# Optimization experiments

Hardware: AMD Instinct MI355X
Metric: run time of the kernel (lower is better)

## Reference

```python
import jax, jax.numpy as jnp
import numpy as np


def setup_inputs() -> dict:
    key = jax.random.key(0)
    k1, k2 = jax.random.split(key)
    latent = jax.random.normal(k1, (131072, 128), dtype=jnp.float32)
    coords = jax.random.normal(k2, (2048, 128), dtype=jnp.float32)
    return {"latent": latent, "coords": coords}


def reference(latent, coords):
    # torch.cdist(latent, coords).min(1)[1]
    # argmin over euclidean distance == argmin over squared distance,
    # so we skip the sqrt (same result, cheaper and numerically safer).
    x2 = jnp.sum(latent * latent, axis=1, keepdims=True)          # [N, 1]
    c2 = jnp.sum(coords * coords, axis=1)                          # [C]
    cross = latent @ coords.T                                      # [N, C]
    d2 = x2 + c2[None, :] - 2.0 * cross                            # [N, C] squared dists
    return jnp.argmin(d2, axis=1)                                  # [N] int indices
```

## Files before the change

kernel.cpp:

```cpp
#include <hip/hip_runtime.h>


constexpr int D = 128;
constexpr int C = 2048;
constexpr int NCH = 32;
constexpr int NCHUNKS = C / NCH;
constexpr float MARGIN_H = 0.01f;
constexpr int WL_CAP = 32768;

constexpr size_t WS_CNT = 16384;
constexpr size_t WS_WL  = 32768;
constexpr size_t WS_BH  = 262144;
constexpr size_t WS_BL  = 524288;

typedef __attribute__((ext_vector_type(4))) int   i32x4;
typedef unsigned int u32;

__device__ __forceinline__ int pack4(int a0, int a1, int a2, int a3) {
    return (int)(((u32)a0 & 255u) | (((u32)a1 & 255u) << 8) |
                 (((u32)a2 & 255u) << 16) | (((u32)a3 & 255u) << 24));
}

__device__ __forceinline__ void q2(float v, float qa, float inv, float inv128,
                                   int* h, int* l) {
    float hf = __builtin_rintf(v * inv);
    *h = (int)hf;
    float r = fmaf(-hf, qa, v);
    *l = (int)__builtin_rintf(r * inv128);
}

__device__ __forceinline__ void gl_lds16(const void* g, void* l) {
    __builtin_amdgcn_global_load_lds(
        (const __attribute__((address_space(1))) u32*)g,
        (__attribute__((address_space(3))) u32*)l, 16, 0, 0);
}

__global__ void prep_coords(const float* __restrict__ coords,
                            signed char* __restrict__ Bh,
                            signed char* __restrict__ Bl,
                            float2* __restrict__ qc2, int* __restrict__ counter) {
    int t = blockIdx.x * blockDim.x + threadIdx.x;
    if (t == 0) *counter = 0;
    if (t >= C * 4) return;
    int c = t >> 2, p = t & 3;
    float v[32];
#pragma unroll
    for (int i = 0; i < 8; ++i)
        *(float4*)(v + i * 4) = *(const float4*)(coords + (size_t)c * D + p * 32 + i * 4);
    float amax = 0.f, ss = 0.f;
#pragma unroll
    for (int j = 0; j < 32; ++j) {
        amax = fmaxf(amax, fabsf(v[j]));
        ss = fmaf(v[j], v[j], ss);
    }
#pragma unroll
    for (int m = 1; m <= 2; m <<= 1) {
        amax = fmaxf(amax, __shfl_xor(amax, m, 64));
        ss += __shfl_xor(ss, m, 64);
    }
    float qb = fmaxf(amax, 1e-30f) * (1.f / 127.f);
    float inv = 127.f / fmaxf(amax, 1e-30f);
    float inv128 = inv * 128.f;

#pragma unroll
    for (int g = 0; g < 2; ++g) {
        int g8 = p * 2 + g;
        int hw[4], lw[4];
#pragma unroll
        for (int w = 0; w < 4; ++w) {
            int h0, l0, h1, l1, h2, l2, h3, l3;
            q2(v[g * 16 + w * 4 + 0], qb, inv, inv128, &h0, &l0);
            q2(v[g * 16 + w * 4 + 1], qb, inv, inv128, &h1, &l1);
            q2(v[g * 16 + w * 4 + 2], qb, inv, inv128, &h2, &l2);
            q2(v[g * 16 + w * 4 + 3], qb, inv, inv128, &h3, &l3);
            hw[w] = pack4(h0, h1, h2, h3);
            lw[w] = pack4(l0, l1, l2, l3);
        }
        size_t off = (size_t)c * 128 + (size_t)((g8 ^ (c & 7)) * 16);
        *(i32x4*)(Bh + off) = (i32x4){hw[0], hw[1], hw[2], hw[3]};
        *(i32x4*)(Bl + off) = (i32x4){lw[0], lw[1], lw[2], lw[3]};
    }
    if (p == 0) qc2[c] = make_float2(qb, -0.5f * ss);
}


__global__ __launch_bounds__(256, 4) void centroid_fast(
        const float* __restrict__ latent,
        const signed char* __restrict__ Bh_img,
        const signed char* __restrict__ Bl_img,
        const float2* __restrict__ qc2g,
        int* __restrict__ out,
        int* __restrict__ counter,
        int* __restrict__ worklist) {
    __shared__ __align__(16) signed char Bh[2][NCH * 128], Bl[2][NCH * 128];
    __shared__ __align__(16) float2 sqc[C];

    const int tid  = threadIdx.x;
    const int wid  = tid >> 6;
    const int lane = tid & 63;
    const int q    = lane >> 4, lr = lane & 15;
    const int row_block = blockIdx.x * 64;

    {
        int ph = (blockIdx.x ^ (blockIdx.x >> 8)) & 3;
        for (int i = 0; i < ph * 2; ++i) __builtin_amdgcn_s_sleep(8);
    }

    gl_lds16(Bh_img + tid * 16, &Bh[0][tid * 16]);
    gl_lds16(Bl_img + tid * 16, &Bl[0][tid * 16]);
#pragma unroll
    for (int i = 0; i < 4; ++i) {
        int off = (i * 256 + tid) * 16;
        gl_lds16((const char*)qc2g + off, (char*)sqc + off);
    }

    i32x4 Ah[2], Al[2];
    float qAr[4];
    {
        const float* rp = latent + (size_t)(row_block + wid * 16 + lr) * D;
        float v[32];
#pragma unroll
        for (int ks = 0; ks < 2; ++ks)
#pragma unroll
            for (int i = 0; i < 4; ++i)
                *(float4*)(v + ks * 16 + i * 4) =
                    *(const float4*)(rp + ks * 64 + q * 16 + i * 4);
        float amax = 0.f;
#pragma unroll
        for (int j = 0; j < 32; ++j) amax = fmaxf(amax, fabsf(v[j]));
        amax = fmaxf(amax, __shfl_xor(amax, 16, 64));
        amax = fmaxf(amax, __shfl_xor(amax, 32, 64));
        float qa = fmaxf(amax, 1e-30f) * (1.f / 127.f);
        float inv = 127.f / fmaxf(amax, 1e-30f);
        float inv128 = inv * 128.f;
#pragma unroll
        for (int ks = 0; ks < 2; ++ks) {
            int hw[4], lw[4];
#pragma unroll
            for (int w = 0; w < 4; ++w) {
                int h0, l0, h1, l1, h2, l2, h3, l3;
                q2(v[ks * 16 + w * 4 + 0], qa, inv, inv128, &h0, &l0);
                q2(v[ks * 16 + w * 4 + 1], qa, inv, inv128, &h1, &l1);
                q2(v[ks * 16 + w * 4 + 2], qa, inv, inv128, &h2, &l2);
                q2(v[ks * 16 + w * 4 + 3], qa, inv, inv128, &h3, &l3);
                hw[w] = pack4(h0, h1, h2, h3);
                lw[w] = pack4(l0, l1, l2, l3);
            }
            Ah[ks] = (i32x4){hw[0], hw[1], hw[2], hw[3]};
            Al[ks] = (i32x4){lw[0], lw[1], lw[2], lw[3]};
        }
#pragma unroll
        for (int r = 0; r < 4; ++r)
            qAr[r] = __shfl(qa, (lane & 48) | (q * 4 + r), 64);
    }

    float b1[4], b2[4];
    int   bidx[4];
#pragma unroll
    for (int s = 0; s < 4; ++s) { b1[s] = -3.4e38f; b2[s] = -3.4e38f; bidx[s] = 0; }

    __syncthreads();

    for (int ch = 0; ch < NCHUNKS; ++ch) {
        const int buf = ch & 1;
        const int chbase = ch * NCH;
        if (ch + 1 < NCHUNKS) {
            const signed char* sh = Bh_img + (size_t)(ch + 1) * (NCH * 128);
            const signed char* sl = Bl_img + (size_t)(ch + 1) * (NCH * 128);
            gl_lds16(sh + tid * 16, &Bh[buf ^ 1][tid * 16]);
            gl_lds16(sl + tid * 16, &Bl[buf ^ 1][tid * 16]);
            asm volatile("s_waitcnt vmcnt(2)" ::: "memory");
        } else {
            asm volatile("s_waitcnt vmcnt(0)" ::: "memory");
        }
        __builtin_amdgcn_s_barrier();

#pragma unroll
        for (int nt = 0; nt < 2; ++nt) {
            const int nl = nt * 16 + lr;
            const float2 qc = sqc[chbase + nl];
            i32x4 I1 = (i32x4){0, 0, 0, 0};
            i32x4 I2 = (i32x4){0, 0, 0, 0};
            __builtin_amdgcn_s_setprio(1);
#pragma unroll
            for (int ks = 0; ks < 2; ++ks) {
                const int e = nl * 128 + (((ks << 2) | q) ^ (lr & 7)) * 16;
                i32x4 bh = *(const i32x4*)(&Bh[buf][e]);
                i32x4 bl = *(const i32x4*)(&Bl[buf][e]);
                I1 = __builtin_amdgcn_mfma_i32_16x16x64_i8(Ah[ks], bh, I1, 0, 0, 0);
                I2 = __builtin_amdgcn_mfma_i32_16x16x64_i8(Ah[ks], bl, I2, 0, 0, 0);
                I2 = __builtin_amdgcn_mfma_i32_16x16x64_i8(Al[ks], bh, I2, 0, 0, 0);
            }
            __builtin_amdgcn_s_setprio(0);
            const int n_global = chbase + nl;
#pragma unroll
            for (int r = 0; r < 4; ++r) {
                float x = fmaf((float)I2[r], 0.0078125f, (float)I1[r]);
                float a = fmaf(qAr[r], x * qc.x, qc.y);
                b2[r]   = __builtin_amdgcn_fmed3f(a, b1[r], b2[r]);
                bool gt = a > b1[r];
                b1[r]   = fmaxf(a, b1[r]);
                bidx[r] = gt ? n_global : bidx[r];
            }
        }
        __builtin_amdgcn_s_barrier();
    }

#pragma unroll
    for (int m = 1; m <= 8; m <<= 1) {
#pragma unroll
        for (int s = 0; s < 4; ++s) {
            float oa = __shfl_xor(b1[s], m, 64);
            float ob = __shfl_xor(b2[s], m, 64);
            int   oi = __shfl_xor(bidx[s], m, 64);
            float mn = fminf(b1[s], oa);
            b2[s] = fmaxf(fmaxf(b2[s], ob), mn);
            bool take = oa > b1[s];
            b1[s]   = take ? oa : b1[s];
            bidx[s] = take ? oi : bidx[s];
        }
    }
#pragma unroll
    for (int s = 0; s < 4; ++s) {
        if (lr == s) {
            int row = row_block + wid * 16 + q * 4 + s;
            out[row] = bidx[s];
            if (b1[s] - b2[s] < MARGIN_H) {
                int w = atomicAdd(counter, 1);
                if (w < WL_CAP) worklist[w] = row;
            }
        }
    }
}


__global__ __launch_bounds__(1024) void refine_fp64(
        const float* __restrict__ latent, const float* __restrict__ coords,
        const int* __restrict__ worklist, const int* __restrict__ counter,
        int wl_cap, int* __restrict__ out) {
    __shared__ float  xs[D];
    __shared__ double rv[1024];
    __shared__ int    ri[1024];

    int n = *counter;
    if (n > wl_cap) n = wl_cap;

    for (int wi = blockIdx.x; wi < n; wi += gridDim.x) {
        int row = worklist[wi];
        if (threadIdx.x < D)
            xs[threadIdx.x] = latent[(size_t)row * D + threadIdx.x];
        __syncthreads();

        double best = 1.0e300;
        int    bix  = 0;
        for (int c = threadIdx.x; c < C; c += 1024) {
            const float4* cp = (const float4*)(coords + (size_t)c * D);
            double s0 = 0.0, s1 = 0.0, s2 = 0.0, s3 = 0.0;
#pragma unroll 8
            for (int k4 = 0; k4 < 32; ++k4) {
                float4 v = cp[k4];
                double d0 = (double)xs[k4 * 4 + 0] - (double)v.x;
                double d1 = (double)xs[k4 * 4 + 1] - (double)v.y;
                double d2 = (double)xs[k4 * 4 + 2] - (double)v.z;
                double d3 = (double)xs[k4 * 4 + 3] - (double)v.w;
                s0 = fma(d0, d0, s0); s1 = fma(d1, d1, s1);
                s2 = fma(d2, d2, s2); s3 = fma(d3, d3, s3);
            }
            double s = (s0 + s1) + (s2 + s3);
            if (s < best) { best = s; bix = c; }
        }
        rv[threadIdx.x] = best;
        ri[threadIdx.x] = bix;
        __syncthreads();
        for (int off = 512; off > 0; off >>= 1) {
            if (threadIdx.x < off) {
                double ov = rv[threadIdx.x + off];
                int    oi = ri[threadIdx.x + off];
                if (ov < rv[threadIdx.x] ||
                    (ov == rv[threadIdx.x] && oi < ri[threadIdx.x])) {
                    rv[threadIdx.x] = ov;
                    ri[threadIdx.x] = oi;
                }
            }
            __syncthreads();
        }
        if (threadIdx.x == 0) out[row] = ri[0];
        __syncthreads();
    }
}

extern "C" void kernel_launch(void* const* d_in, const int* in_sizes, int n_in,
                              void* d_out, int out_size, void* d_ws, size_t ws_size,
                              hipStream_t stream) {
    const float* latent = (const float*)d_in[0];
    const float* coords = (const float*)d_in[1];
    int*         out    = (int*)d_out;

    char* ws = (char*)d_ws;
    float2* qc2    = (float2*)ws;
    int*    counter = (int*)(ws + WS_CNT);
    int*    wl      = (int*)(ws + WS_WL);
    signed char* Bh = (signed char*)(ws + WS_BH);
    signed char* Bl = (signed char*)(ws + WS_BL);
    const int n_rows = in_sizes[0] / D;

    prep_coords<<<(C * 4) / 256, 256, 0, stream>>>(coords, Bh, Bl, qc2, counter);
    centroid_fast<<<n_rows / 64, 256, 0, stream>>>(latent, Bh, Bl, qc2, out,
                                                   counter, wl);
    refine_fp64<<<608, 1024, 0, stream>>>(latent, coords, wl, counter, WL_CAP, out);
}
```

Baseline: 279.8 us.

## Use global quantization scales so distance scoring runs in pure integer arithmetic

Replaces the per-row and per-centroid int8 quantization scales with a single global absolute-max scale for each of latent and coords, computed by a new pre-pass kernel. With shared scales, the -0.5·||c||² term becomes a scaled integer bias folded into the MFMA accumulator, and the score and top-2 tracking run as integer ops instead of float conversions and FMAs. The ambiguity margin becomes an integer threshold, and the chunk size doubles to 64 centroids. The trade-offs are a full extra read of the latent matrix for the global max and coarser quantization, which can push more rows into the fp64 refine pass.

```diff
diff --git a/kernel.cpp b/kernel.cpp
--- a/kernel.cpp
+++ b/kernel.cpp
@@ -3,17 +3,17 @@
 
 constexpr int D = 128;
 constexpr int C = 2048;
-constexpr int NCH = 32;
+constexpr int NCH = 64;
 constexpr int NCHUNKS = C / NCH;
-constexpr float MARGIN_H = 0.01f;
 constexpr int WL_CAP = 32768;
 
 constexpr size_t WS_CNT = 16384;
 constexpr size_t WS_WL  = 32768;
+constexpr size_t WS_V   = 196608;
 constexpr size_t WS_BH  = 262144;
 constexpr size_t WS_BL  = 524288;
 
-typedef __attribute__((ext_vector_type(4))) int   i32x4;
+typedef __attribute__((ext_vector_type(4))) int i32x4;
 typedef unsigned int u32;
 
 __device__ __forceinline__ int pack4(int a0, int a1, int a2, int a3) {
@@ -35,32 +35,57 @@
         (__attribute__((address_space(3))) u32*)l, 16, 0, 0);
 }
 
+__global__ void prep_amax(const float* __restrict__ latent, int nA4,
+                          const float* __restrict__ coords, int nB4,
+                          unsigned* __restrict__ amax, int* __restrict__ counter) {
+    int t = blockIdx.x * blockDim.x + threadIdx.x;
+    if (t == 0) *counter = 0;
+    int stride = gridDim.x * blockDim.x;
+    float mA = 0.f, mB = 0.f;
+    for (int i = t; i < nA4; i += stride) {
+        float4 v = ((const float4*)latent)[i];
+        mA = fmaxf(mA, fmaxf(fmaxf(fabsf(v.x), fabsf(v.y)),
+                             fmaxf(fabsf(v.z), fabsf(v.w))));
+    }
+    for (int i = t; i < nB4; i += stride) {
+        float4 v = ((const float4*)coords)[i];
+        mB = fmaxf(mB, fmaxf(fmaxf(fabsf(v.x), fabsf(v.y)),
+                             fmaxf(fabsf(v.z), fabsf(v.w))));
+    }
+#pragma unroll
+    for (int m = 1; m <= 32; m <<= 1) {
+        mA = fmaxf(mA, __shfl_xor(mA, m, 64));
+        mB = fmaxf(mB, __shfl_xor(mB, m, 64));
+    }
+    if ((threadIdx.x & 63) == 0) {
+        atomicMax(amax + 0, __float_as_uint(mA));
+        atomicMax(amax + 1, __float_as_uint(mB));
+    }
+}
+
 __global__ void prep_coords(const float* __restrict__ coords,
+                            const unsigned* __restrict__ amax,
                             signed char* __restrict__ Bh,
                             signed char* __restrict__ Bl,
-                            float2* __restrict__ qc2, int* __restrict__ counter) {
+                            int* __restrict__ Vt) {
     int t = blockIdx.x * blockDim.x + threadIdx.x;
-    if (t == 0) *counter = 0;
     if (t >= C * 4) return;
     int c = t >> 2, p = t & 3;
+    float aA = fmaxf(__uint_as_float(amax[0]), 1e-30f);
+    float aB = fmaxf(__uint_as_float(amax[1]), 1e-30f);
+    float qb = aB * (1.f / 127.f);
+    float inv = 127.f / aB;
+    float inv128 = inv * 128.f;
+
     float v[32];
 #pragma unroll
     for (int i = 0; i < 8; ++i)
         *(float4*)(v + i * 4) = *(const float4*)(coords + (size_t)c * D + p * 32 + i * 4);
-    float amax = 0.f, ss = 0.f;
-#pragma unroll
-    for (int j = 0; j < 32; ++j) {
-        amax = fmaxf(amax, fabsf(v[j]));
-        ss = fmaf(v[j], v[j], ss);
-    }
-#pragma unroll
-    for (int m = 1; m <= 2; m <<= 1) {
-        amax = fmaxf(amax, __shfl_xor(amax, m, 64));
-        ss += __shfl_xor(ss, m, 64);
-    }
-    float qb = fmaxf(amax, 1e-30f) * (1.f / 127.f);
-    float inv = 127.f / fmaxf(amax, 1e-30f);
-    float inv128 = inv * 128.f;
+    float ss = 0.f;
+#pragma unroll
+    for (int j = 0; j < 32; ++j) ss = fmaf(v[j], v[j], ss);
+#pragma unroll
+    for (int m = 1; m <= 2; m <<= 1) ss += __shfl_xor(ss, m, 64);
 
 #pragma unroll
     for (int g = 0; g < 2; ++g) {
@@ -80,7 +105,10 @@
         *(i32x4*)(Bh + off) = (i32x4){hw[0], hw[1], hw[2], hw[3]};
         *(i32x4*)(Bl + off) = (i32x4){lw[0], lw[1], lw[2], lw[3]};
     }
-    if (p == 0) qc2[c] = make_float2(qb, -0.5f * ss);
+    if (p == 0) {
+        float sAB = aA * aB * (1.f / 16129.f);
+        Vt[c] = (int)rintf(-64.f * ss / sAB);
+    }
 }
 
 
@@ -88,12 +116,13 @@
         const float* __restrict__ latent,
         const signed char* __restrict__ Bh_img,
         const signed char* __restrict__ Bl_img,
-        const float2* __restrict__ qc2g,
+        const int* __restrict__ Vg,
+        const unsigned* __restrict__ amax,
         int* __restrict__ out,
         int* __restrict__ counter,
         int* __restrict__ worklist) {
     __shared__ __align__(16) signed char Bh[2][NCH * 128], Bl[2][NCH * 128];
-    __shared__ __align__(16) float2 sqc[C];
+    __shared__ __align__(16) int Vs[C];
 
     const int tid  = threadIdx.x;
     const int wid  = tid >> 6;
@@ -106,58 +135,56 @@
         for (int i = 0; i < ph * 2; ++i) __builtin_amdgcn_s_sleep(8);
     }
 
-    gl_lds16(Bh_img + tid * 16, &Bh[0][tid * 16]);
-    gl_lds16(Bl_img + tid * 16, &Bl[0][tid * 16]);
-#pragma unroll
-    for (int i = 0; i < 4; ++i) {
+#pragma unroll
+    for (int i = 0; i < 2; ++i) {
+        int e = (i * 256 + tid) * 16;
+        gl_lds16(Bh_img + e, &Bh[0][e]);
+        gl_lds16(Bl_img + e, &Bl[0][e]);
+    }
+#pragma unroll
+    for (int i = 0; i < 2; ++i) {
         int off = (i * 256 + tid) * 16;
-        gl_lds16((const char*)qc2g + off, (char*)sqc + off);
-    }
+        gl_lds16((const char*)Vg + off, (char*)Vs + off);
+    }
+
+    const float aA = fmaxf(__uint_as_float(amax[0]), 1e-30f);
+    const float aB = fmaxf(__uint_as_float(amax[1]), 1e-30f);
+    const float sAB = aA * aB * (1.f / 16129.f);
+    const int M_int = (int)(1.28f / sAB) + 1;
 
     i32x4 Ah[2], Al[2];
-    float qAr[4];
     {
         const float* rp = latent + (size_t)(row_block + wid * 16 + lr) * D;
-        float v[32];
-#pragma unroll
-        for (int ks = 0; ks < 2; ++ks)
+        float qa = aA * (1.f / 127.f);
+        float inv = 127.f / aA;
+        float inv128 = inv * 128.f;
+#pragma unroll
+        for (int ks = 0; ks < 2; ++ks) {
+            float v[16];
 #pragma unroll
             for (int i = 0; i < 4; ++i)
-                *(float4*)(v + ks * 16 + i * 4) =
-                    *(const float4*)(rp + ks * 64 + q * 16 + i * 4);
-        float amax = 0.f;
-#pragma unroll
-        for (int j = 0; j < 32; ++j) amax = fmaxf(amax, fabsf(v[j]));
-        amax = fmaxf(amax, __shfl_xor(amax, 16, 64));
-        amax = fmaxf(amax, __shfl_xor(amax, 32, 64));
-        float qa = fmaxf(amax, 1e-30f) * (1.f / 127.f);
-        float inv = 127.f / fmaxf(amax, 1e-30f);
-        float inv128 = inv * 128.f;
-#pragma unroll
-        for (int ks = 0; ks < 2; ++ks) {
+                *(float4*)(v + i * 4) = *(const float4*)(rp + ks * 64 + q * 16 + i * 4);
             int hw[4], lw[4];
 #pragma unroll
             for (int w = 0; w < 4; ++w) {
                 int h0, l0, h1, l1, h2, l2, h3, l3;
-                q2(v[ks * 16 + w * 4 + 0], qa, inv, inv128, &h0, &l0);
-                q2(v[ks * 16 + w * 4 + 1], qa, inv, inv128, &h1, &l1);
-                q2(v[ks * 16 + w * 4 + 2], qa, inv, inv128, &h2, &l2);
-                q2(v[ks * 16 + w * 4 + 3], qa, inv, inv128, &h3, &l3);
+                q2(v[w * 4 + 0], qa, inv, inv128, &h0, &l0);
+                q2(v[w * 4 + 1], qa, inv, inv128, &h1, &l1);
+                q2(v[w * 4 + 2], qa, inv, inv128, &h2, &l2);
+                q2(v[w * 4 + 3], qa, inv, inv128, &h3, &l3);
                 hw[w] = pack4(h0, h1, h2, h3);
                 lw[w] = pack4(l0, l1, l2, l3);
             }
             Ah[ks] = (i32x4){hw[0], hw[1], hw[2], hw[3]};
             Al[ks] = (i32x4){lw[0], lw[1], lw[2], lw[3]};
         }
-#pragma unroll
-        for (int r = 0; r < 4; ++r)
-            qAr[r] = __shfl(qa, (lane & 48) | (q * 4 + r), 64);
-    }
-
-    float b1[4], b2[4];
-    int   bidx[4];
-#pragma unroll
-    for (int s = 0; s < 4; ++s) { b1[s] = -3.4e38f; b2[s] = -3.4e38f; bidx[s] = 0; }
+    }
+
+    int b1[4], b2[4], bidx[4];
+#pragma unroll
+    for (int s = 0; s < 4; ++s) {
+        b1[s] = -2147483647 - 1; b2[s] = -2147483647 - 1; bidx[s] = 0;
+    }
 
     __syncthreads();
 
@@ -167,20 +194,24 @@
         if (ch + 1 < NCHUNKS) {
             const signed char* sh = Bh_img + (size_t)(ch + 1) * (NCH * 128);
             const signed char* sl = Bl_img + (size_t)(ch + 1) * (NCH * 128);
-            gl_lds16(sh + tid * 16, &Bh[buf ^ 1][tid * 16]);
-            gl_lds16(sl + tid * 16, &Bl[buf ^ 1][tid * 16]);
-            asm volatile("s_waitcnt vmcnt(2)" ::: "memory");
+#pragma unroll
+            for (int i = 0; i < 2; ++i) {
+                int e = (i * 256 + tid) * 16;
+                gl_lds16(sh + e, &Bh[buf ^ 1][e]);
+                gl_lds16(sl + e, &Bl[buf ^ 1][e]);
+            }
+            asm volatile("s_waitcnt vmcnt(4)" ::: "memory");
         } else {
             asm volatile("s_waitcnt vmcnt(0)" ::: "memory");
         }
         __builtin_amdgcn_s_barrier();
 
 #pragma unroll
-        for (int nt = 0; nt < 2; ++nt) {
+        for (int nt = 0; nt < 4; ++nt) {
             const int nl = nt * 16 + lr;
-            const float2 qc = sqc[chbase + nl];
+            const int v0 = Vs[chbase + nl];
             i32x4 I1 = (i32x4){0, 0, 0, 0};
-            i32x4 I2 = (i32x4){0, 0, 0, 0};
+            i32x4 I2 = (i32x4){v0, v0, v0, v0};
             __builtin_amdgcn_s_setprio(1);
 #pragma unroll
             for (int ks = 0; ks < 2; ++ks) {
@@ -195,11 +226,10 @@
             const int n_global = chbase + nl;
 #pragma unroll
             for (int r = 0; r < 4; ++r) {
-                float x = fmaf((float)I2[r], 0.0078125f, (float)I1[r]);
-                float a = fmaf(qAr[r], x * qc.x, qc.y);
-                b2[r]   = __builtin_amdgcn_fmed3f(a, b1[r], b2[r]);
-                bool gt = a > b1[r];
-                b1[r]   = fmaxf(a, b1[r]);
+                int S = (int)(((u32)I1[r] << 7) + (u32)I2[r]);
+                bool gt = S > b1[r];
+                b2[r]   = max(b2[r], min(S, b1[r]));
+                b1[r]   = max(S, b1[r]);
                 bidx[r] = gt ? n_global : bidx[r];
             }
         }
@@ -210,11 +240,11 @@
     for (int m = 1; m <= 8; m <<= 1) {
 #pragma unroll
         for (int s = 0; s < 4; ++s) {
-            float oa = __shfl_xor(b1[s], m, 64);
-            float ob = __shfl_xor(b2[s], m, 64);
-            int   oi = __shfl_xor(bidx[s], m, 64);
-            float mn = fminf(b1[s], oa);
-            b2[s] = fmaxf(fmaxf(b2[s], ob), mn);
+            int oa = __shfl_xor(b1[s], m, 64);
+            int ob = __shfl_xor(b2[s], m, 64);
+            int oi = __shfl_xor(bidx[s], m, 64);
+            int mn = min(b1[s], oa);
+            b2[s] = max(max(b2[s], ob), mn);
             bool take = oa > b1[s];
             b1[s]   = take ? oa : b1[s];
             bidx[s] = take ? oi : bidx[s];
@@ -225,7 +255,7 @@
         if (lr == s) {
             int row = row_block + wid * 16 + q * 4 + s;
             out[row] = bidx[s];
-            if (b1[s] - b2[s] < MARGIN_H) {
+            if (b1[s] - b2[s] < M_int) {
                 int w = atomicAdd(counter, 1);
                 if (w < WL_CAP) worklist[w] = row;
             }
@@ -297,15 +327,20 @@
     int*         out    = (int*)d_out;
 
     char* ws = (char*)d_ws;
-    float2* qc2    = (float2*)ws;
+    unsigned* amax  = (unsigned*)ws;
     int*    counter = (int*)(ws + WS_CNT);
     int*    wl      = (int*)(ws + WS_WL);
+    int*    Vt      = (int*)(ws + WS_V);
     signed char* Bh = (signed char*)(ws + WS_BH);
     signed char* Bl = (signed char*)(ws + WS_BL);
     const int n_rows = in_sizes[0] / D;
-
-    prep_coords<<<(C * 4) / 256, 256, 0, stream>>>(coords, Bh, Bl, qc2, counter);
-    centroid_fast<<<n_rows / 64, 256, 0, stream>>>(latent, Bh, Bl, qc2, out,
+    const int nA4 = n_rows * D / 4;
+    const int nB4 = C * D / 4;
+
+    hipMemsetAsync(d_ws, 0, 16, stream);
+    prep_amax<<<1024, 256, 0, stream>>>(latent, nA4, coords, nB4, amax, counter);
+    prep_coords<<<(C * 4) / 256, 256, 0, stream>>>(coords, amax, Bh, Bl, Vt);
+    centroid_fast<<<n_rows / 64, 256, 0, stream>>>(latent, Bh, Bl, Vt, amax, out,
                                                    counter, wl);
     refine_fp64<<<608, 1024, 0, stream>>>(latent, coords, wl, counter, WL_CAP, out);
 }
```

Result: slower. 370.2 us (+32.3%).
